# Optimization experiments

Hardware: AMD Instinct MI355X
Metric: run time of the kernel (lower is better)

The kernel has to match this reference:

```python
import jax, jax.numpy as jnp
import numpy as np

TOKENS = 8192
MODEL_DIM = 4096
PROMPT_DIM = 64
NUM_EXPERTS = 8
TOP_K = 2
EPS = float(np.finfo(np.float32).eps)


def setup_inputs() -> dict:
    key = jax.random.key(0)
    k1, k2, k3 = jax.random.split(key, 3)
    x = jax.random.normal(k1, (TOKENS, MODEL_DIM), dtype=jnp.float32)
    prompt = jax.random.normal(k2, (TOKENS, PROMPT_DIM), dtype=jnp.float32)
    # gate linear: Linear(model_dim + prompt_dim, num_experts, bias=True)
    W = jax.random.normal(k3, (MODEL_DIM + PROMPT_DIM, NUM_EXPERTS), dtype=jnp.float32) * 0.02
    b = jnp.zeros((NUM_EXPERTS,), dtype=jnp.float32)
    return {"x": x, "prompt": prompt, "W": W, "b": b}


def reference(x, prompt, W, b):
    # eval path: no jitter, no noise (self.training is False)
    logits = jnp.concatenate([x, prompt], axis=-1) @ W + b          # [T, E]
    _, topk_idx = jax.lax.top_k(logits, TOP_K)                      # [T, K]
    masks = jax.nn.one_hot(topk_idx, NUM_EXPERTS, dtype=jnp.float32)  # [T, K, E]
    gates = jax.nn.softmax(logits, axis=-1)                         # [T, E]
    gates_s = jnp.einsum("te,tke->tk", gates, masks)               # masked gather-sum
    if TOP_K > 1:
        denom = jnp.maximum(gates_s.sum(axis=-1, keepdims=True), EPS)
        gates_s = gates_s / denom
    # masks[:, i] == masks_se[i], gates_s[:, i] == gates_s[i] in the torch code
    return masks, gates_s
```

## Files before the change

### kernel.cpp

```cpp
#include <hip/hip_runtime.h>
#include <math.h>

#define NE 8
#define KDIM 4096
#define PDIM 64
#define WROWS (KDIM + PDIM)
#define EPS_F32 1.1920929e-07f
#define NCHUNK 16
#define TPW 2

typedef float f4 __attribute__((ext_vector_type(4)));

__global__ __launch_bounds__(256)
void transpose_w(const float* __restrict__ W, float* __restrict__ Wt) {
    const int k = blockIdx.x * 256 + threadIdx.x;
    if (k < WROWS) {
        float v[NE];
#pragma unroll
        for (int e = 0; e < NE; ++e) v[e] = W[(size_t)k * NE + e];
#pragma unroll
        for (int e = 0; e < NE; ++e) Wt[(size_t)e * WROWS + k] = v[e];
    }
}

__global__ __launch_bounds__(64, 4)
void topk_gate(const float* __restrict__ x,
               const float* __restrict__ prompt,
               const float* __restrict__ Wt,
               const float* __restrict__ b,
               float* __restrict__ out,
               int tokens)
{
    const int lane  = threadIdx.x;
    const int tbase = blockIdx.x * TPW;
    const int klane = lane * 4;
    const int phase = (blockIdx.x * 5) & 15;

    float acc[TPW][NE];
#pragma unroll
    for (int t = 0; t < TPW; ++t)
#pragma unroll
        for (int e = 0; e < NE; ++e) acc[t][e] = 0.f;

    const float* xr0 = x + (size_t)tbase * KDIM;
    const float* xr1 = xr0 + KDIM;
    const float* wr[NE];
#pragma unroll
    for (int e = 0; e < NE; ++e)
        wr[e] = Wt + (size_t)e * WROWS;

    f4 xb[3][TPW];
    f4 wb[2][NE];

    auto koff = [&](int c) { return ((c + phase) & 15) * 256 + klane; };

    {
        const int k0 = koff(0);
#pragma unroll
        for (int e = 0; e < NE; ++e)
            wb[0][e] = *(const f4*)(wr[e] + k0);
        xb[0][0] = *(const f4*)(xr0 + k0);
        xb[0][1] = *(const f4*)(xr1 + k0);
        const int k1 = koff(1);
        xb[1][0] = *(const f4*)(xr0 + k1);
        xb[1][1] = *(const f4*)(xr1 + k1);
    }

#pragma unroll
    for (int c = 0; c < NCHUNK; ++c) {
        if (c + 1 < NCHUNK) {
            const int kw = koff(c + 1);
#pragma unroll
            for (int e = 0; e < NE; ++e)
                wb[(c + 1) & 1][e] = *(const f4*)(wr[e] + kw);
        }
        if (c + 2 < NCHUNK) {
            const int kx = koff(c + 2);
            xb[(c + 2) % 3][0] = *(const f4*)(xr0 + kx);
            xb[(c + 2) % 3][1] = *(const f4*)(xr1 + kx);
        }

        const int s = c % 3;
        const int wv = c & 1;
#pragma unroll
        for (int t = 0; t < TPW; ++t)
#pragma unroll
            for (int e = 0; e < NE; ++e) {
                const f4 xv = xb[s][t];
                acc[t][e] = fmaf(xv.x, wb[wv][e].x, acc[t][e]);
                acc[t][e] = fmaf(xv.y, wb[wv][e].y, acc[t][e]);
                acc[t][e] = fmaf(xv.z, wb[wv][e].z, acc[t][e]);
                acc[t][e] = fmaf(xv.w, wb[wv][e].w, acc[t][e]);
            }
    }

    if (lane < 16) {
        const int k = lane * 4;
        f4 pv[TPW];
#pragma unroll
        for (int t = 0; t < TPW; ++t)
            pv[t] = *(const f4*)(prompt + (size_t)(tbase + t) * PDIM + k);
#pragma unroll
        for (int e = 0; e < NE; ++e) {
            const f4 wv = *(const f4*)(Wt + (size_t)e * WROWS + KDIM + k);
#pragma unroll
            for (int t = 0; t < TPW; ++t) {
                acc[t][e] = fmaf(pv[t].x, wv.x, acc[t][e]);
                acc[t][e] = fmaf(pv[t].y, wv.y, acc[t][e]);
                acc[t][e] = fmaf(pv[t].z, wv.z, acc[t][e]);
                acc[t][e] = fmaf(pv[t].w, wv.w, acc[t][e]);
            }
        }
    }

#pragma unroll
    for (int t = 0; t < TPW; ++t)
#pragma unroll
        for (int e = 0; e < NE; ++e) {
            float v = acc[t][e];
#pragma unroll
            for (int off = 32; off >= 1; off >>= 1)
                v += __shfl_xor(v, off, 64);
            acc[t][e] = v;
        }

    const int tt = (lane >> 4) & 1;
    const int kk = (lane >> 3) & 1;
    const int ee = lane & 7;

    float lg[NE];
#pragma unroll
    for (int e = 0; e < NE; ++e) {
        const float v = (tt == 0) ? acc[0][e] : acc[1][e];
        lg[e] = v + b[e];
    }

    float v0 = lg[0]; int i0 = 0;
#pragma unroll
    for (int e = 1; e < NE; ++e)
        if (lg[e] > v0) { v0 = lg[e]; i0 = e; }
    float v1 = (i0 == 0) ? lg[1] : lg[0];
    int   i1 = (i0 == 0) ? 1 : 0;
#pragma unroll
    for (int e = 0; e < NE; ++e)
        if (e != i0 && lg[e] > v1) { v1 = lg[e]; i1 = e; }

    float s = 0.f;
#pragma unroll
    for (int e = 0; e < NE; ++e) s += __expf(lg[e] - v0);
    const float g0 = 1.0f / s;
    const float g1 = __expf(v1 - v0) / s;
    const float denom = fmaxf(g0 + g1, EPS_F32);

    if (lane < 32) {
        const int sel = kk ? i1 : i0;
        const int t_global = tbase + tt;
        out[(size_t)t_global * 16 + kk * 8 + ee] = (ee == sel) ? 1.0f : 0.0f;

        if ((lane & 15) < 2) {
            const float g = (ee == 0) ? (g0 / denom) : (g1 / denom);
            out[(size_t)tokens * 16 + (size_t)t_global * 2 + ee] = g;
        }
    }
}

extern "C" void kernel_launch(void* const* d_in, const int* in_sizes, int n_in,
                              void* d_out, int out_size, void* d_ws, size_t ws_size,
                              hipStream_t stream) {
    const float* x      = (const float*)d_in[0];
    const float* prompt = (const float*)d_in[1];
    const float* W      = (const float*)d_in[2];
    const float* b      = (const float*)d_in[3];
    float* out          = (float*)d_out;
    float* Wt           = (float*)d_ws;

    const int tokens = in_sizes[0] / KDIM;

    hipLaunchKernelGGL(transpose_w, dim3((WROWS + 255) / 256), dim3(256), 0, stream,
                       W, Wt);
    hipLaunchKernelGGL(topk_gate, dim3(tokens / TPW), dim3(64), 0, stream,
                       x, prompt, Wt, b, out, tokens);
}
```

Measured before the change: 215.6 us.

## Stage transposed gate weights in LDS and share across 16 waves per block

```diff
diff --git a/kernel.cpp b/kernel.cpp
--- a/kernel.cpp
+++ b/kernel.cpp
@@ -8,6 +8,9 @@
 #define EPS_F32 1.1920929e-07f
 #define NCHUNK 16
 #define TPW 2
+#define WAVES 16
+#define ROWF4 (WROWS / 4)
+#define LDSF4 (NE * ROWF4)
 
 typedef float f4 __attribute__((ext_vector_type(4)));
 
@@ -23,7 +26,7 @@
     }
 }
 
-__global__ __launch_bounds__(64, 4)
+__global__ __launch_bounds__(1024, 4)
 void topk_gate(const float* __restrict__ x,
                const float* __restrict__ prompt,
                const float* __restrict__ Wt,
@@ -31,9 +34,20 @@
                float* __restrict__ out,
                int tokens)
 {
-    const int lane  = threadIdx.x;
-    const int tbase = blockIdx.x * TPW;
-    const int klane = lane * 4;
+    __shared__ f4 wlds[LDSF4];
+
+    const int tid  = threadIdx.x;
+    const int lane = tid & 63;
+    const int wid  = tid >> 6;
+
+    {
+        const f4* wt4 = (const f4*)Wt;
+        for (int i = tid; i < LDSF4; i += WAVES * 64)
+            wlds[i] = wt4[i];
+    }
+    __syncthreads();
+
+    const int tbase = (blockIdx.x * WAVES + wid) * TPW;
     const int phase = (blockIdx.x * 5) & 15;
 
     float acc[TPW][NE];
@@ -42,67 +56,57 @@
 #pragma unroll
         for (int e = 0; e < NE; ++e) acc[t][e] = 0.f;
 
-    const float* xr0 = x + (size_t)tbase * KDIM;
-    const float* xr1 = xr0 + KDIM;
-    const float* wr[NE];
-#pragma unroll
-    for (int e = 0; e < NE; ++e)
-        wr[e] = Wt + (size_t)e * WROWS;
+    const f4* xr0 = (const f4*)(x + (size_t)tbase * KDIM);
+    const f4* xr1 = (const f4*)(x + (size_t)(tbase + 1) * KDIM);
 
     f4 xb[3][TPW];
-    f4 wb[2][NE];
 
-    auto koff = [&](int c) { return ((c + phase) & 15) * 256 + klane; };
+    auto cidx = [&](int c) { return ((c + phase) & 15) * 64 + lane; };
 
     {
-        const int k0 = koff(0);
-#pragma unroll
-        for (int e = 0; e < NE; ++e)
-            wb[0][e] = *(const f4*)(wr[e] + k0);
-        xb[0][0] = *(const f4*)(xr0 + k0);
-        xb[0][1] = *(const f4*)(xr1 + k0);
-        const int k1 = koff(1);
-        xb[1][0] = *(const f4*)(xr0 + k1);
-        xb[1][1] = *(const f4*)(xr1 + k1);
+        const int k0 = cidx(0);
+        xb[0][0] = __builtin_nontemporal_load(xr0 + k0);
+        xb[0][1] = __builtin_nontemporal_load(xr1 + k0);
+        const int k1 = cidx(1);
+        xb[1][0] = __builtin_nontemporal_load(xr0 + k1);
+        xb[1][1] = __builtin_nontemporal_load(xr1 + k1);
     }
 
 #pragma unroll
     for (int c = 0; c < NCHUNK; ++c) {
-        if (c + 1 < NCHUNK) {
-            const int kw = koff(c + 1);
-#pragma unroll
-            for (int e = 0; e < NE; ++e)
-                wb[(c + 1) & 1][e] = *(const f4*)(wr[e] + kw);
-        }
         if (c + 2 < NCHUNK) {
-            const int kx = koff(c + 2);
-            xb[(c + 2) % 3][0] = *(const f4*)(xr0 + kx);
-            xb[(c + 2) % 3][1] = *(const f4*)(xr1 + kx);
+            const int kx = cidx(c + 2);
+            xb[(c + 2) % 3][0] = __builtin_nontemporal_load(xr0 + kx);
+            xb[(c + 2) % 3][1] = __builtin_nontemporal_load(xr1 + kx);
         }
 
+        const int kw = cidx(c);
+        f4 wb[NE];
+#pragma unroll
+        for (int e = 0; e < NE; ++e)
+            wb[e] = wlds[e * ROWF4 + kw];
+
         const int s = c % 3;
-        const int wv = c & 1;
 #pragma unroll
         for (int t = 0; t < TPW; ++t)
 #pragma unroll
             for (int e = 0; e < NE; ++e) {
                 const f4 xv = xb[s][t];
-                acc[t][e] = fmaf(xv.x, wb[wv][e].x, acc[t][e]);
-                acc[t][e] = fmaf(xv.y, wb[wv][e].y, acc[t][e]);
-                acc[t][e] = fmaf(xv.z, wb[wv][e].z, acc[t][e]);
-                acc[t][e] = fmaf(xv.w, wb[wv][e].w, acc[t][e]);
+                acc[t][e] = fmaf(xv.x, wb[e].x, acc[t][e]);
+                acc[t][e] = fmaf(xv.y, wb[e].y, acc[t][e]);
+                acc[t][e] = fmaf(xv.z, wb[e].z, acc[t][e]);
+                acc[t][e] = fmaf(xv.w, wb[e].w, acc[t][e]);
             }
     }
 
     if (lane < 16) {
-        const int k = lane * 4;
         f4 pv[TPW];
 #pragma unroll
         for (int t = 0; t < TPW; ++t)
-            pv[t] = *(const f4*)(prompt + (size_t)(tbase + t) * PDIM + k);
+            pv[t] = *((const f4*)(prompt + (size_t)(tbase + t) * PDIM) + lane);
 #pragma unroll
         for (int e = 0; e < NE; ++e) {
-            const f4 wv = *(const f4*)(Wt + (size_t)e * WROWS + KDIM + k);
+            const f4 wv = wlds[e * ROWF4 + (KDIM / 4) + lane];
 #pragma unroll
             for (int t = 0; t < TPW; ++t) {
                 acc[t][e] = fmaf(pv[t].x, wv.x, acc[t][e]);
@@ -178,6 +182,6 @@
 
     hipLaunchKernelGGL(transpose_w, dim3((WROWS + 255) / 256), dim3(256), 0, stream,
                        W, Wt);
-    hipLaunchKernelGGL(topk_gate, dim3(tokens / TPW), dim3(64), 0, stream,
-                       x, prompt, Wt, b, out, tokens);
+    hipLaunchKernelGGL(topk_gate, dim3(tokens / (WAVES * TPW)), dim3(WAVES * 64),
+                       0, stream, x, prompt, Wt, b, out, tokens);
 }
```

After: 202.4 us. -6.1%, faster.
